# Performance work log

Hardware: AMD Instinct MI355X
Metric: run time of the kernel (lower is better)

## Reference

```python
import jax, jax.numpy as jnp
import numpy as np

EPS_COS = 1e-8
EPS_SHARP = 1e-16


def setup_inputs() -> dict:
    key = jax.random.key(0)
    k1, k2, k3, k4 = jax.random.split(key, 4)
    B, H, R, C, M = 512, 512, 2048, 64, 3
    out_dim = 3 * C + 2 * M + 4  # 202
    h = jax.random.normal(k1, (B, H), dtype=jnp.float32)
    prev_w = jax.random.uniform(k2, (B, R), dtype=jnp.float32)
    prev_w = prev_w / prev_w.sum(axis=1, keepdims=True)  # valid focus distribution
    memory = jax.random.normal(k3, (B, R, C), dtype=jnp.float32)
    fc_w = jax.random.normal(k4, (out_dim, H), dtype=jnp.float32) * 0.05
    fc_b = jnp.zeros((out_dim,), dtype=jnp.float32)
    return {"h": h, "prev_w": prev_w, "memory": memory, "fc_w": fc_w, "fc_b": fc_b}


def _write_head(h, prev_w, memory, fc_w, fc_b):
    B, R, C = memory.shape
    total = fc_w.shape[0]
    shift_len = total - 3 * C - 3          # 2*max_shift + 1
    m = (shift_len - 1) // 2               # max_shift

    z = h @ fc_w.T + fc_b                  # [B, total]
    sizes = [C, 1, 1, shift_len, 1, C, C]
    offs = np.cumsum([0] + sizes)
    k     = jnp.tanh(z[:, offs[0]:offs[1]])                 # [B, C]
    beta  = jax.nn.softplus(z[:, offs[1]:offs[2]])          # [B, 1]
    g     = jax.nn.sigmoid(z[:, offs[2]:offs[3]])           # [B, 1]
    s     = jax.nn.softmax(z[:, offs[3]:offs[4]], axis=1)   # [B, 2m+1]
    gamma = jax.nn.softplus(z[:, offs[4]:offs[5]]) + 1.0    # [B, 1]
    e     = jax.nn.sigmoid(z[:, offs[5]:offs[6]])           # [B, C]
    a     = jnp.tanh(z[:, offs[6]:offs[7]])                 # [B, C]

    # content addressing: cosine similarity of k vs each memory row
    num = jnp.einsum('bc,brc->br', k, memory)
    k_n = jnp.maximum(jnp.linalg.norm(k, axis=1, keepdims=True), EPS_COS)   # [B,1]
    m_n = jnp.maximum(jnp.linalg.norm(memory, axis=2), EPS_COS)             # [B,R]
    w_c = jax.nn.softmax(beta * (num / (k_n * m_n)), axis=1)                # [B,R]

    # gated interpolation
    w_g = g * w_c + (1.0 - g) * prev_w                                      # [B,R]

    # circular shift (per-sample cross-correlation, O(B*R*(2m+1)))
    unrolled = jnp.concatenate([w_g[:, -m:], w_g, w_g[:, :m]], axis=1)      # [B, R+2m]
    windows = jnp.stack([unrolled[:, j:j + R] for j in range(2 * m + 1)], axis=1)  # [B,2m+1,R]
    w_s = jnp.einsum('bjr,bj->br', windows, s)                              # [B,R]

    # sharpen
    w_p = jnp.power(w_s, gamma)
    w = w_p / (w_p.sum(axis=1, keepdims=True) + EPS_SHARP)                  # [B,R]

    # erase + write (fused)
    wE = w[:, :, None]                                                      # [B,R,1]
    new_mem = memory * (1.0 - wE * e[:, None, :]) + wE * a[:, None, :]      # [B,R,C]
    return w, new_mem


def reference(h, prev_w, memory, fc_w, fc_b):
    return _write_head(h, prev_w, memory, fc_w, fc_b)
```

## Files before the change

### kernel.cpp

```cpp
#include <hip/hip_runtime.h>
#include <math.h>

#define BB 512
#define HH 512
#define RR 2048
#define CC 64
#define OUTD 202
#define PSTRIDE 208
#define K_OFF 0
#define E_OFF 64
#define A_OFF 128
#define S_OFF 192
#define COMBO_OFF 199
#define G_OFF 200
#define GAMMA_OFF 201

#define PART_STRIDE 224

typedef float f32x4 __attribute__((ext_vector_type(4)));

__device__ __forceinline__ float softplusf_(float x) {
    return (x > 20.f) ? x : log1pf(expf(x));
}
__device__ __forceinline__ float sigmoidf_(float x) {
    return 1.f / (1.f + expf(-x));
}

__global__ __launch_bounds__(256) void params_part_kernel(
    const float* __restrict__ h, const float* __restrict__ fc_w,
    float* __restrict__ part)
{
    __shared__ float h_sh[8][128];
    const int tid = threadIdx.x;
    const int bg = blockIdx.x >> 2;
    const int hq = blockIdx.x & 3;
    const int b0 = bg * 8;
    const int h0 = hq * 128;

    for (int idx = tid; idx < 8 * 128; idx += 256) {
        int j = idx >> 7, i = idx & 127;
        h_sh[j][i] = h[(size_t)(b0 + j) * HH + h0 + i];
    }
    __syncthreads();

    if (tid < OUTD) {
        float acc[8];
        #pragma unroll
        for (int j = 0; j < 8; ++j) acc[j] = 0.f;
        const float4* wr = (const float4*)(fc_w + (size_t)tid * HH + h0);
        #pragma unroll 4
        for (int i4 = 0; i4 < 32; ++i4) {
            float4 wv = wr[i4];
            int i = i4 * 4;
            #pragma unroll
            for (int j = 0; j < 8; ++j) {
                acc[j] = fmaf(wv.x, h_sh[j][i + 0], acc[j]);
                acc[j] = fmaf(wv.y, h_sh[j][i + 1], acc[j]);
                acc[j] = fmaf(wv.z, h_sh[j][i + 2], acc[j]);
                acc[j] = fmaf(wv.w, h_sh[j][i + 3], acc[j]);
            }
        }
        #pragma unroll
        for (int j = 0; j < 8; ++j) {
            part[((size_t)(b0 + j) * 4 + hq) * PART_STRIDE + tid] = acc[j];
        }
    }
}

__global__ __launch_bounds__(256) void params_combine_kernel(
    const float* __restrict__ part, const float* __restrict__ fc_b,
    float* __restrict__ pw)
{
    __shared__ float z_sh[80];
    const int b = blockIdx.x;
    const int tid = threadIdx.x;
    float* p = pw + (size_t)b * PSTRIDE;

    if (tid < OUTD) {
        const float* q = part + (size_t)b * 4 * PART_STRIDE + tid;
        float z = q[0] + q[PART_STRIDE] + q[2 * PART_STRIDE]
                + q[3 * PART_STRIDE] + fc_b[tid];
        if (tid < 74) z_sh[tid] = z;
        if (tid < 64)                      p[K_OFF + tid] = tanhf(z);
        else if (tid == 65)                p[G_OFF] = sigmoidf_(z);
        else if (tid == 73)                p[GAMMA_OFF] = softplusf_(z) + 1.f;
        else if (tid >= 74 && tid < 138)   p[E_OFF + (tid - 74)] = sigmoidf_(z);
        else if (tid >= 138)               p[A_OFF + (tid - 138)] = tanhf(z);
    }
    __syncthreads();

    if (tid < 64) {
        float kv = tanhf(z_sh[tid]);
        float ss = kv * kv;
        #pragma unroll
        for (int m = 1; m < 64; m <<= 1) ss += __shfl_xor(ss, m, 64);
        if (tid == 0) {
            float kn = fmaxf(sqrtf(ss), 1e-8f);
            float beta = softplusf_(z_sh[64]);
            p[COMBO_OFF] = beta / kn;
            float mx = -1e30f;
            #pragma unroll
            for (int q = 0; q < 7; ++q) mx = fmaxf(mx, z_sh[66 + q]);
            float ev[7], se = 0.f;
            #pragma unroll
            for (int q = 0; q < 7; ++q) {
                ev[q] = __expf(z_sh[66 + q] - mx);
                se += ev[q];
            }
            float inv = 1.f / se;
            #pragma unroll
            for (int q = 0; q < 7; ++q) p[S_OFF + q] = ev[q] * inv;
        }
    }
}

__device__ __forceinline__ float block_reduce_sum4(float v, float* red) {
    #pragma unroll
    for (int m = 1; m < 64; m <<= 1) v += __shfl_xor(v, m, 64);
    int wid = threadIdx.x >> 6;
    if ((threadIdx.x & 63) == 0) red[wid] = v;
    __syncthreads();
    float x = red[0] + red[1] + red[2] + red[3];
    __syncthreads();
    return x;
}

__global__ __launch_bounds__(256) void score_kernel(
    const float* __restrict__ memory, const float* __restrict__ pw,
    float* __restrict__ sc, float* __restrict__ esum)
{
    __shared__ float red[4];
    const int tid = threadIdx.x;
    const int b = blockIdx.x >> 2;
    const int rbase = (blockIdx.x & 3) * 512;
    const int lane16 = tid & 15;
    const int rgrp = tid >> 4;
    const float* p = pw + (size_t)b * PSTRIDE;
    const float4 k4 = *(const float4*)(p + K_OFF + lane16 * 4);
    const float combo = p[COMBO_OFF];
    const float* memb = memory + (size_t)b * RR * CC;

    float lsum = 0.f;
    #pragma unroll 8
    for (int i = 0; i < 32; ++i) {
        int r = rbase + i * 16 + rgrp;
        float4 m4 = *(const float4*)(memb + (size_t)r * CC + lane16 * 4);
        float num = m4.x * k4.x + m4.y * k4.y + m4.z * k4.z + m4.w * k4.w;
        float ssq = m4.x * m4.x + m4.y * m4.y + m4.z * m4.z + m4.w * m4.w;
        #pragma unroll
        for (int m = 1; m < 16; m <<= 1) {
            num += __shfl_xor(num, m, 64);
            ssq += __shfl_xor(ssq, m, 64);
        }
        if (lane16 == 0) {
            float mn = fmaxf(sqrtf(ssq), 1e-8f);
            float ev = __expf(combo * num / mn);
            sc[(size_t)b * RR + r] = ev;
            lsum += ev;
        }
    }
    float bs = block_reduce_sum4(lsum, red);
    if (tid == 0) esum[blockIdx.x] = bs;
}

__global__ __launch_bounds__(256) void weight_kernel(
    const float* __restrict__ sc, const float* __restrict__ esum,
    const float* __restrict__ prev_w, const float* __restrict__ pw,
    float* __restrict__ out_w)
{
    __shared__ float buf[RR];
    __shared__ float wg[RR];
    __shared__ float red[4];
    const int b = blockIdx.x;
    const int tid = threadIdx.x;
    const float* p = pw + (size_t)b * PSTRIDE;
    const float g = p[G_OFF];
    const float gamma = p[GAMMA_OFF];
    const float s0 = p[S_OFF + 0], s1 = p[S_OFF + 1], s2 = p[S_OFF + 2],
                s3 = p[S_OFF + 3], s4 = p[S_OFF + 4], s5 = p[S_OFF + 5],
                s6 = p[S_OFF + 6];
    const float* eb = esum + (size_t)b * 4;
    const float se = eb[0] + eb[1] + eb[2] + eb[3];
    const float gi = g / se, omg = 1.f - g;

    #pragma unroll
    for (int t = 0; t < 4; ++t) {
        int r2 = (t * 256 + tid) * 2;
        float2 ev = *(const float2*)(sc + (size_t)b * RR + r2);
        float2 pv = *(const float2*)(prev_w + (size_t)b * RR + r2);
        wg[r2]     = gi * ev.x + omg * pv.x;
        wg[r2 + 1] = gi * ev.y + omg * pv.y;
    }
    __syncthreads();

    float lp = 0.f;
    #pragma unroll
    for (int t = 0; t < 8; ++t) {
        int r = t * 256 + tid;
        float acc = s0 * wg[(r - 3) & (RR - 1)]
                  + s1 * wg[(r - 2) & (RR - 1)]
                  + s2 * wg[(r - 1) & (RR - 1)]
                  + s3 * wg[r]
                  + s4 * wg[(r + 1) & (RR - 1)]
                  + s5 * wg[(r + 2) & (RR - 1)]
                  + s6 * wg[(r + 3) & (RR - 1)];
        float v = __powf(acc, gamma);
        buf[r] = v;
        lp += v;
    }
    const float ps = block_reduce_sum4(lp, red);
    const float invp = 1.f / (ps + 1e-16f);

    #pragma unroll
    for (int t = 0; t < 4; ++t) {
        int r2 = (t * 256 + tid) * 2;
        *(float2*)(out_w + (size_t)b * RR + r2) =
            make_float2(buf[r2] * invp, buf[r2 + 1] * invp);
    }
}

__global__ __launch_bounds__(256) void update_kernel(
    const float* __restrict__ memory, const float* __restrict__ w,
    const float* __restrict__ pw, float* __restrict__ out_mem)
{
    const int bid = (int)gridDim.x - 1 - (int)blockIdx.x;
    const int b = bid >> 2;
    const int rbase = (bid & 3) * 512;
    const int tid = threadIdx.x;
    const int lane8 = tid & 7;
    const int rgrp = tid >> 3;
    const float* p = pw + (size_t)b * PSTRIDE;
    const f32x4 ea = *(const f32x4*)(p + E_OFF + lane8 * 8);
    const f32x4 eb2 = *(const f32x4*)(p + E_OFF + lane8 * 8 + 4);
    const f32x4 aa = *(const f32x4*)(p + A_OFF + lane8 * 8);
    const f32x4 ab = *(const f32x4*)(p + A_OFF + lane8 * 8 + 4);
    const float* memb = memory + (size_t)b * RR * CC;
    float* omb = out_mem + (size_t)b * RR * CC;
    const float* wb = w + (size_t)b * RR;

    #pragma unroll
    for (int mi = 0; mi < 4; ++mi) {
        f32x4 ma[4], mb[4];
        float wv[4];
        #pragma unroll
        for (int j = 0; j < 4; ++j) {
            int r = rbase + (mi * 4 + j) * 32 + rgrp;
            const f32x4* mp = (const f32x4*)(memb + (size_t)r * CC + lane8 * 8);
            ma[j] = mp[0];
            mb[j] = mp[1];
            wv[j] = wb[r];
        }
        #pragma unroll
        for (int j = 0; j < 4; ++j) {
            int r = rbase + (mi * 4 + j) * 32 + rgrp;
            f32x4 oa, ob;
            oa.x = ma[j].x * (1.f - wv[j] * ea.x) + wv[j] * aa.x;
            oa.y = ma[j].y * (1.f - wv[j] * ea.y) + wv[j] * aa.y;
            oa.z = ma[j].z * (1.f - wv[j] * ea.z) + wv[j] * aa.z;
            oa.w = ma[j].w * (1.f - wv[j] * ea.w) + wv[j] * aa.w;
            ob.x = mb[j].x * (1.f - wv[j] * eb2.x) + wv[j] * ab.x;
            ob.y = mb[j].y * (1.f - wv[j] * eb2.y) + wv[j] * ab.y;
            ob.z = mb[j].z * (1.f - wv[j] * eb2.z) + wv[j] * ab.z;
            ob.w = mb[j].w * (1.f - wv[j] * eb2.w) + wv[j] * ab.w;
            f32x4* op = (f32x4*)(omb + (size_t)r * CC + lane8 * 8);
            op[0] = oa;
            op[1] = ob;
        }
    }
}

extern "C" void kernel_launch(void* const* d_in, const int* in_sizes, int n_in,
                              void* d_out, int out_size, void* d_ws, size_t ws_size,
                              hipStream_t stream) {
    const float* h      = (const float*)d_in[0];
    const float* prev_w = (const float*)d_in[1];
    const float* memory = (const float*)d_in[2];
    const float* fc_w   = (const float*)d_in[3];
    const float* fc_b   = (const float*)d_in[4];

    float* pw      = (float*)d_ws;
    float* out_w   = (float*)d_out;
    float* out_mem = out_w + (size_t)BB * RR;

    const size_t pw_f   = (size_t)BB * PSTRIDE;
    const size_t br_f   = (size_t)BB * RR;
    const size_t es_f   = (size_t)BB * 4;
    const size_t part_f = (size_t)BB * 4 * PART_STRIDE;
    const size_t need_f = pw_f + br_f + es_f + part_f;

    float* sc   = pw + pw_f;
    float* esum = sc + br_f;
    float* part = esum + es_f;

    if (ws_size >= need_f * sizeof(float)) {
        params_part_kernel<<<256, 256, 0, stream>>>(h, fc_w, part);
        params_combine_kernel<<<BB, 256, 0, stream>>>(part, fc_b, pw);
        score_kernel<<<BB * 4, 256, 0, stream>>>(memory, pw, sc, esum);
        weight_kernel<<<BB, 256, 0, stream>>>(sc, esum, prev_w, pw, out_w);
        update_kernel<<<BB * 4, 256, 0, stream>>>(memory, out_w, pw, out_mem);
    } else {
        float* sc_fb   = out_mem;
        float* esum_fb = pw + pw_f;
        float* part_fb = esum_fb + es_f;
        params_part_kernel<<<256, 256, 0, stream>>>(h, fc_w, part_fb);
        params_combine_kernel<<<BB, 256, 0, stream>>>(part_fb, fc_b, pw);
        score_kernel<<<BB * 4, 256, 0, stream>>>(memory, pw, sc_fb, esum_fb);
        weight_kernel<<<BB, 256, 0, stream>>>(sc_fb, esum_fb, prev_w, pw, out_w);
        update_kernel<<<BB * 4, 256, 0, stream>>>(memory, out_w, pw, out_mem);
    }
}
```

Before: 188.8 us.

## Fuse score, weighting and memory update into one cooperative grid-synced kernel

Replaces the three separate score, weight and update launches with one cooperative kernel of 1024 blocks. Each block handles half of one batch row's memory, and grid-wide syncs separate the softmax-normalisation and sharpening reductions. The aim is to cut launch gaps and the separate weight pass, and to reuse recently read memory rows from cache in the update phase. The cost is two grid barriers and the requirement that all blocks be co-resident; it falls back to the old kernels if the cooperative launch is unsupported or fails, or if the workspace is too small, and that fallback path no longer places its buffers in the output when the workspace is short.

```diff
diff --git a/kernel.cpp b/kernel.cpp
--- a/kernel.cpp
+++ b/kernel.cpp
@@ -1,5 +1,8 @@
 #include <hip/hip_runtime.h>
+#include <hip/hip_cooperative_groups.h>
 #include <math.h>
+
+namespace cg = cooperative_groups;
 
 #define BB 512
 #define HH 512
@@ -123,6 +126,139 @@
     float x = red[0] + red[1] + red[2] + red[3];
     __syncthreads();
     return x;
+}
+
+__global__ __launch_bounds__(256, 4) void coop_kernel(
+    const float* __restrict__ memory, const float* __restrict__ prev_w,
+    const float* __restrict__ pw, float* __restrict__ sc,
+    float* __restrict__ esum, float* __restrict__ wp,
+    float* __restrict__ psum, float* __restrict__ out_w,
+    float* __restrict__ out_mem)
+{
+    cg::grid_group grid = cg::this_grid();
+    __shared__ float wgs[1030];
+    __shared__ float red[4];
+
+    const int tid = threadIdx.x;
+    const int bid = blockIdx.x;
+    const int b = bid >> 1;
+    const int rbase = (bid & 1) * 1024;
+    const float* p = pw + (size_t)b * PSTRIDE;
+    const float* memb = memory + (size_t)b * RR * CC;
+
+    {
+        const int lane16 = tid & 15;
+        const int rgrp = tid >> 4;
+        const float4 k4 = *(const float4*)(p + K_OFF + lane16 * 4);
+        const float combo = p[COMBO_OFF];
+        float lsum = 0.f;
+        #pragma unroll 8
+        for (int i = 0; i < 64; ++i) {
+            int r = rbase + i * 16 + rgrp;
+            float4 m4 = *(const float4*)(memb + (size_t)r * CC + lane16 * 4);
+            float num = m4.x * k4.x + m4.y * k4.y + m4.z * k4.z + m4.w * k4.w;
+            float ssq = m4.x * m4.x + m4.y * m4.y + m4.z * m4.z + m4.w * m4.w;
+            #pragma unroll
+            for (int m = 1; m < 16; m <<= 1) {
+                num += __shfl_xor(num, m, 64);
+                ssq += __shfl_xor(ssq, m, 64);
+            }
+            if (lane16 == 0) {
+                float mn = fmaxf(sqrtf(ssq), 1e-8f);
+                float ev = __expf(combo * num / mn);
+                sc[(size_t)b * RR + r] = ev;
+                lsum += ev;
+            }
+        }
+        float bs = block_reduce_sum4(lsum, red);
+        if (tid == 0) esum[bid] = bs;
+    }
+    grid.sync();
+
+    const float g = p[G_OFF];
+    const float gamma = p[GAMMA_OFF];
+    {
+        const float s0 = p[S_OFF + 0], s1 = p[S_OFF + 1], s2 = p[S_OFF + 2],
+                    s3 = p[S_OFF + 3], s4 = p[S_OFF + 4], s5 = p[S_OFF + 5],
+                    s6 = p[S_OFF + 6];
+        const float se = esum[2 * b] + esum[2 * b + 1];
+        const float gi = g / se, omg = 1.f - g;
+
+        for (int idx = tid; idx < 1030; idx += 256) {
+            int r = (rbase - 3 + idx) & (RR - 1);
+            wgs[idx] = gi * sc[(size_t)b * RR + r]
+                     + omg * prev_w[(size_t)b * RR + r];
+        }
+        __syncthreads();
+
+        float lp = 0.f;
+        #pragma unroll
+        for (int t = 0; t < 4; ++t) {
+            int idx = t * 256 + tid;
+            float acc = s0 * wgs[idx]     + s1 * wgs[idx + 1]
+                      + s2 * wgs[idx + 2] + s3 * wgs[idx + 3]
+                      + s4 * wgs[idx + 4] + s5 * wgs[idx + 5]
+                      + s6 * wgs[idx + 6];
+            float v = __powf(acc, gamma);
+            wp[(size_t)b * RR + rbase + idx] = v;
+            lp += v;
+        }
+        float bs = block_reduce_sum4(lp, red);
+        if (tid == 0) psum[bid] = bs;
+    }
+    grid.sync();
+
+    {
+        const float invp = 1.f / (psum[2 * b] + psum[2 * b + 1] + 1e-16f);
+        const float* wpb = wp + (size_t)b * RR;
+
+        #pragma unroll
+        for (int t = 0; t < 2; ++t) {
+            int r2 = rbase + (t * 256 + tid) * 2;
+            float2 wv2 = *(const float2*)(wpb + r2);
+            *(float2*)(out_w + (size_t)b * RR + r2) =
+                make_float2(wv2.x * invp, wv2.y * invp);
+        }
+
+        const int lane8 = tid & 7;
+        const int rgrp = tid >> 3;
+        const f32x4 ea = *(const f32x4*)(p + E_OFF + lane8 * 8);
+        const f32x4 eb2 = *(const f32x4*)(p + E_OFF + lane8 * 8 + 4);
+        const f32x4 aa = *(const f32x4*)(p + A_OFF + lane8 * 8);
+        const f32x4 ab = *(const f32x4*)(p + A_OFF + lane8 * 8 + 4);
+        float* omb = out_mem + (size_t)b * RR * CC;
+
+        #pragma unroll
+        for (int mi = 0; mi < 8; ++mi) {
+            f32x4 ma[4], mb[4];
+            float wv[4];
+            #pragma unroll
+            for (int j = 0; j < 4; ++j) {
+                int r = rbase + (mi * 4 + j) * 32 + rgrp;
+                const f32x4* mp =
+                    (const f32x4*)(memb + (size_t)r * CC + lane8 * 8);
+                ma[j] = mp[0];
+                mb[j] = mp[1];
+                wv[j] = wpb[r] * invp;
+            }
+            #pragma unroll
+            for (int j = 0; j < 4; ++j) {
+                int r = rbase + (mi * 4 + j) * 32 + rgrp;
+                f32x4 oa, ob;
+                oa.x = ma[j].x * (1.f - wv[j] * ea.x) + wv[j] * aa.x;
+                oa.y = ma[j].y * (1.f - wv[j] * ea.y) + wv[j] * aa.y;
+                oa.z = ma[j].z * (1.f - wv[j] * ea.z) + wv[j] * aa.z;
+                oa.w = ma[j].w * (1.f - wv[j] * ea.w) + wv[j] * aa.w;
+                ob.x = mb[j].x * (1.f - wv[j] * eb2.x) + wv[j] * ab.x;
+                ob.y = mb[j].y * (1.f - wv[j] * eb2.y) + wv[j] * ab.y;
+                ob.z = mb[j].z * (1.f - wv[j] * eb2.z) + wv[j] * ab.z;
+                ob.w = mb[j].w * (1.f - wv[j] * eb2.w) + wv[j] * ab.w;
+                f32x4* op = (f32x4*)(omb + (size_t)r * CC + lane8 * 8);
+                op[0] = oa;
+                op[1] = ob;
+            }
+        }
+    }
 }
 
 __global__ __launch_bounds__(256) void score_kernel(
@@ -286,26 +422,37 @@
     const size_t br_f   = (size_t)BB * RR;
     const size_t es_f   = (size_t)BB * 4;
     const size_t part_f = (size_t)BB * 4 * PART_STRIDE;
-    const size_t need_f = pw_f + br_f + es_f + part_f;
+    const size_t need_f = pw_f + 2 * br_f + 2 * es_f + part_f;
 
     float* sc   = pw + pw_f;
-    float* esum = sc + br_f;
-    float* part = esum + es_f;
-
-    if (ws_size >= need_f * sizeof(float)) {
-        params_part_kernel<<<256, 256, 0, stream>>>(h, fc_w, part);
-        params_combine_kernel<<<BB, 256, 0, stream>>>(part, fc_b, pw);
+    float* wp   = sc + br_f;
+    float* esum = wp + br_f;
+    float* psum = esum + es_f;
+    float* part = psum + es_f;
+
+    params_part_kernel<<<256, 256, 0, stream>>>(h, fc_w, part);
+    params_combine_kernel<<<BB, 256, 0, stream>>>(part, fc_b, pw);
+
+    int coop_attr = 0;
+    int dev = 0;
+    hipGetDevice(&dev);
+    hipDeviceGetAttribute(&coop_attr, hipDeviceAttributeCooperativeLaunch, dev);
+
+    bool coop_ok = coop_attr && (ws_size >= need_f * sizeof(float));
+    if (coop_ok) {
+        void* args[] = {
+            (void*)&memory, (void*)&prev_w, (void*)&pw, (void*)&sc,
+            (void*)&esum, (void*)&wp, (void*)&psum, (void*)&out_w,
+            (void*)&out_mem
+        };
+        hipError_t e = hipLaunchCooperativeKernel(
+            (const void*)coop_kernel, dim3(BB * 2), dim3(256), args, 0, stream);
+        if (e != hipSuccess) coop_ok = false;
+    }
+
+    if (!coop_ok) {
         score_kernel<<<BB * 4, 256, 0, stream>>>(memory, pw, sc, esum);
         weight_kernel<<<BB, 256, 0, stream>>>(sc, esum, prev_w, pw, out_w);
         update_kernel<<<BB * 4, 256, 0, stream>>>(memory, out_w, pw, out_mem);
-    } else {
-        float* sc_fb   = out_mem;
-        float* esum_fb = pw + pw_f;
-        float* part_fb = esum_fb + es_f;
-        params_part_kernel<<<256, 256, 0, stream>>>(h, fc_w, part_fb);
-        params_combine_kernel<<<BB, 256, 0, stream>>>(part_fb, fc_b, pw);
-        score_kernel<<<BB * 4, 256, 0, stream>>>(memory, pw, sc_fb, esum_fb);
-        weight_kernel<<<BB, 256, 0, stream>>>(sc_fb, esum_fb, prev_w, pw, out_w);
-        update_kernel<<<BB * 4, 256, 0, stream>>>(memory, out_w, pw, out_mem);
-    }
-}
+    }
+}
```

Measured after the change: 416.4 us. 2.21x slower.
